# Optimization experiments

Hardware: AMD Instinct MI355X
Metric: run time of the kernel (lower is better)

The kernel has to match this reference:

```python
import jax, jax.numpy as jnp
import numpy as np

S, B, C = 7, 2, 20
D = C + 5 * B  # 30
LAMBDA_COORD = 5.0
LAMBDA_NOOBJ = 0.5
EPS = 1e-6


def _iou_yolo(b1, b2):
    # b1, b2: [..., 4] boxes in (cx, cy, w, h) 'yolo' format
    b1x1 = b1[..., 0] - b1[..., 2] / 2
    b1y1 = b1[..., 1] - b1[..., 3] / 2
    b1x2 = b1[..., 0] + b1[..., 2] / 2
    b1y2 = b1[..., 1] + b1[..., 3] / 2
    b2x1 = b2[..., 0] - b2[..., 2] / 2
    b2y1 = b2[..., 1] - b2[..., 3] / 2
    b2x2 = b2[..., 0] + b2[..., 2] / 2
    b2y2 = b2[..., 1] + b2[..., 3] / 2
    iw = jnp.clip(jnp.minimum(b1x2, b2x2) - jnp.maximum(b1x1, b2x1), 0.0)
    ih = jnp.clip(jnp.minimum(b1y2, b2y2) - jnp.maximum(b1y1, b2y1), 0.0)
    inter = iw * ih
    a1 = jnp.abs((b1x2 - b1x1) * (b1y2 - b1y1))
    a2 = jnp.abs((b2x2 - b2x1) * (b2y2 - b2y1))
    return inter / (a1 + a2 - inter + EPS)


def setup_inputs() -> dict:
    batch = 16384
    key = jax.random.key(0)
    k1, k2, k3 = jax.random.split(key, 3)
    # true coords / classes in (0.05, 0.95) so sqrt(w), sqrt(h) are well-defined
    y_trues = jax.random.uniform(k1, (batch, S, S, D), dtype=jnp.float32) * 0.9 + 0.05
    conf = (jax.random.uniform(k2, (batch, S, S)) < 0.3).astype(jnp.float32)
    y_trues = y_trues.at[..., 4].set(conf)  # objectness indicator is exactly 0 or 1
    y_preds = jax.random.normal(k3, (batch, S, S, D), dtype=jnp.float32)
    return {"y_trues": y_trues, "y_preds": y_preds}


def reference(y_trues, y_preds):
    yt = y_trues.reshape(-1, S * S, D)
    yp = y_preds.reshape(-1, S * S, D)
    batch = yt.shape[0]

    obj = (yt[..., 4] == 1.0).astype(yt.dtype)   # [N, S*S]
    noobj = 1.0 - obj

    iou1 = _iou_yolo(yt[..., 0:4], yp[..., 0:4])
    iou2 = _iou_yolo(yt[..., 0:4], yp[..., 5:9])
    best1 = iou1 > iou2                           # responsible box selection

    box_hat = jnp.where(best1[..., None], yp[..., 0:4], yp[..., 5:9])
    conf_hat = jnp.where(best1, yp[..., 4], yp[..., 9])        # responsible conf
    other_conf_hat = jnp.where(best1, yp[..., 9], yp[..., 4])  # non-responsible conf

    # xy offset loss
    xy = (yt[..., 0] - box_hat[..., 0]) ** 2 + (yt[..., 1] - box_hat[..., 1]) ** 2
    # wh loss: sqrt(true) vs sqrt(|pred + eps|)
    wh = (jnp.sqrt(yt[..., 2]) - jnp.sqrt(jnp.abs(box_hat[..., 2] + EPS))) ** 2 \
       + (jnp.sqrt(yt[..., 3]) - jnp.sqrt(jnp.abs(box_hat[..., 3] + EPS))) ** 2
    # object confidence loss (true conf == 1 in obj cells)
    obj_conf = (yt[..., 4] - conf_hat) ** 2
    # no-object penalty on the NON-responsible box inside object cells (target 0)
    noobj_in_obj = LAMBDA_NOOBJ * other_conf_hat ** 2
    # no-object penalty on BOTH boxes in cells without objects (true conf == 0)
    noobj_cells = LAMBDA_NOOBJ * ((yt[..., 4] - yp[..., 4]) ** 2
                                  + (yt[..., 4] - yp[..., 9]) ** 2)
    # class loss over C classes
    cls = jnp.sum((yt[..., 10:] - yp[..., 10:]) ** 2, axis=-1)

    per_cell = obj * (LAMBDA_COORD * (xy + wh) + obj_conf + noobj_in_obj + cls) \
             + noobj * noobj_cells
    return jnp.sum(per_cell) / batch
```

## Files before the change

### kernel.cpp

```cpp
#include <hip/hip_runtime.h>


#define SS 49
#define DD 30

__device__ __forceinline__ float iou_yolo(const float b1[4], const float b2[4]) {
    const float EPS = 1e-6f;
    float b1x1 = b1[0] - b1[2] * 0.5f, b1y1 = b1[1] - b1[3] * 0.5f;
    float b1x2 = b1[0] + b1[2] * 0.5f, b1y2 = b1[1] + b1[3] * 0.5f;
    float b2x1 = b2[0] - b2[2] * 0.5f, b2y1 = b2[1] - b2[3] * 0.5f;
    float b2x2 = b2[0] + b2[2] * 0.5f, b2y2 = b2[1] + b2[3] * 0.5f;
    float iw = fmaxf(fminf(b1x2, b2x2) - fmaxf(b1x1, b2x1), 0.0f);
    float ih = fmaxf(fminf(b1y2, b2y2) - fmaxf(b1y1, b2y1), 0.0f);
    float inter = iw * ih;
    float a1 = fabsf((b1x2 - b1x1) * (b1y2 - b1y1));
    float a2 = fabsf((b2x2 - b2x1) * (b2y2 - b2y1));
    return inter / (a1 + a2 - inter + EPS);
}

__global__ __launch_bounds__(256)
void yolo_loss_kernel(const float* __restrict__ yt_g,
                      const float* __restrict__ yp_g,
                      float* __restrict__ out,
                      int ncells, float inv_batch) {
    const float LAMBDA_COORD = 5.0f;
    const float LAMBDA_NOOBJ = 0.5f;
    const float EPS = 1e-6f;

    int cell = blockIdx.x * blockDim.x + threadIdx.x;
    float per_cell = 0.0f;

    if (cell < ncells) {
        const float2* yt2 = reinterpret_cast<const float2*>(yt_g + (size_t)cell * DD);
        const float2* yp2 = reinterpret_cast<const float2*>(yp_g + (size_t)cell * DD);
        float yt[DD], yp[DD];
#pragma unroll
        for (int i = 0; i < DD / 2; ++i) {
            float2 a = yt2[i]; yt[2 * i] = a.x; yt[2 * i + 1] = a.y;
            float2 b = yp2[i]; yp[2 * i] = b.x; yp[2 * i + 1] = b.y;
        }

        float obj = (yt[4] == 1.0f) ? 1.0f : 0.0f;
        float noobj = 1.0f - obj;

        float iou1 = iou_yolo(&yt[0], &yp[0]);
        float iou2 = iou_yolo(&yt[0], &yp[5]);
        bool best1 = iou1 > iou2;

        float bh0 = best1 ? yp[0] : yp[5];
        float bh1 = best1 ? yp[1] : yp[6];
        float bh2 = best1 ? yp[2] : yp[7];
        float bh3 = best1 ? yp[3] : yp[8];
        float conf_hat       = best1 ? yp[4] : yp[9];
        float other_conf_hat = best1 ? yp[9] : yp[4];

        float dx = yt[0] - bh0, dy = yt[1] - bh1;
        float xy = dx * dx + dy * dy;

        float sw = sqrtf(yt[2]) - sqrtf(fabsf(bh2 + EPS));
        float sh = sqrtf(yt[3]) - sqrtf(fabsf(bh3 + EPS));
        float wh = sw * sw + sh * sh;

        float dc = yt[4] - conf_hat;
        float obj_conf = dc * dc;

        float noobj_in_obj = LAMBDA_NOOBJ * other_conf_hat * other_conf_hat;

        float d4 = yt[4] - yp[4];
        float d9 = yt[4] - yp[9];
        float noobj_cells = LAMBDA_NOOBJ * (d4 * d4 + d9 * d9);

        float cls = 0.0f;
#pragma unroll
        for (int k = 10; k < DD; ++k) {
            float d = yt[k] - yp[k];
            cls += d * d;
        }

        per_cell = obj * (LAMBDA_COORD * (xy + wh) + obj_conf + noobj_in_obj + cls)
                 + noobj * noobj_cells;
    }

#pragma unroll
    for (int off = 32; off > 0; off >>= 1)
        per_cell += __shfl_down(per_cell, off, 64);

    __shared__ float smem[4];
    int lane = threadIdx.x & 63;
    int wave = threadIdx.x >> 6;
    if (lane == 0) smem[wave] = per_cell;
    __syncthreads();
    if (threadIdx.x == 0) {
        float s = smem[0] + smem[1] + smem[2] + smem[3];
        atomicAdd(out, s * inv_batch);
    }
}

extern "C" void kernel_launch(void* const* d_in, const int* in_sizes, int n_in,
                              void* d_out, int out_size, void* d_ws, size_t ws_size,
                              hipStream_t stream) {
    const float* yt = (const float*)d_in[0];
    const float* yp = (const float*)d_in[1];
    float* out = (float*)d_out;

    int total = in_sizes[0];
    int ncells = total / DD;
    int batch = ncells / SS;

    hipMemsetAsync(out, 0, sizeof(float), stream);

    int block = 256;
    int grid = (ncells + block - 1) / block;
    yolo_loss_kernel<<<grid, block, 0, stream>>>(yt, yp, out, ncells, 1.0f / (float)batch);
}
```

Measured before the change: 211.7 us.

## Stage cell tiles into LDS with coalesced direct global-to-LDS loads

Each block now copies its contiguous tile of 256 cells for both inputs into shared memory using 16-byte global_load_lds transfers, then each thread reads its cell's 30 floats from LDS. Previously each thread issued strided float2 loads at a 120-byte stride, which coalesce poorly. The cost is 60 KB of LDS per block, which limits occupancy, an extra barrier, and LDS bank conflicts from the stride-30 per-thread reads.

```diff
diff --git a/kernel.cpp b/kernel.cpp
--- a/kernel.cpp
+++ b/kernel.cpp
@@ -3,6 +3,16 @@
 
 #define SS 49
 #define DD 30
+#define BLOCK 256
+#define CPB 256
+#define TILE_F (CPB * DD)
+
+__device__ __forceinline__ void g2l16(const float* g, float* l) {
+    __builtin_amdgcn_global_load_lds(
+        (const __attribute__((address_space(1))) void*)g,
+        (__attribute__((address_space(3))) void*)l,
+        16, 0, 0);
+}
 
 __device__ __forceinline__ float iou_yolo(const float b1[4], const float b2[4]) {
     const float EPS = 1e-6f;
@@ -18,7 +28,7 @@
     return inter / (a1 + a2 - inter + EPS);
 }
 
-__global__ __launch_bounds__(256)
+__global__ __launch_bounds__(BLOCK)
 void yolo_loss_kernel(const float* __restrict__ yt_g,
                       const float* __restrict__ yp_g,
                       float* __restrict__ out,
@@ -27,24 +37,42 @@
     const float LAMBDA_NOOBJ = 0.5f;
     const float EPS = 1e-6f;
 
-    int cell = blockIdx.x * blockDim.x + threadIdx.x;
+    __shared__ __align__(16) float lt[TILE_F];
+    __shared__ __align__(16) float lp[TILE_F];
+
+    const int tid = threadIdx.x;
+    const int base_cell = blockIdx.x * CPB;
+    const int nc = min(CPB, ncells - base_cell);
+    const int nf = nc * DD;
+    const int nf4 = nf >> 2;
+    const size_t base_f = (size_t)base_cell * DD;
+
+    const float* gt = yt_g + base_f;
+    const float* gp = yp_g + base_f;
+
+    for (int j = tid; j < nf4; j += BLOCK) {
+        g2l16(gt + 4 * j, &lt[4 * j]);
+        g2l16(gp + 4 * j, &lp[4 * j]);
+    }
+    for (int j = (nf4 << 2) + tid; j < nf; j += BLOCK) {
+        lt[j] = gt[j];
+        lp[j] = gp[j];
+    }
+    __syncthreads();
+
     float per_cell = 0.0f;
-
-    if (cell < ncells) {
-        const float2* yt2 = reinterpret_cast<const float2*>(yt_g + (size_t)cell * DD);
-        const float2* yp2 = reinterpret_cast<const float2*>(yp_g + (size_t)cell * DD);
-        float yt[DD], yp[DD];
-#pragma unroll
-        for (int i = 0; i < DD / 2; ++i) {
-            float2 a = yt2[i]; yt[2 * i] = a.x; yt[2 * i + 1] = a.y;
-            float2 b = yp2[i]; yp[2 * i] = b.x; yp[2 * i + 1] = b.y;
-        }
+    if (tid < nc) {
+        const float* yt = &lt[tid * DD];
+        const float* yp = &lp[tid * DD];
 
         float obj = (yt[4] == 1.0f) ? 1.0f : 0.0f;
         float noobj = 1.0f - obj;
 
-        float iou1 = iou_yolo(&yt[0], &yp[0]);
-        float iou2 = iou_yolo(&yt[0], &yp[5]);
+        float tb[4] = {yt[0], yt[1], yt[2], yt[3]};
+        float pb1[4] = {yp[0], yp[1], yp[2], yp[3]};
+        float pb2[4] = {yp[5], yp[6], yp[7], yp[8]};
+        float iou1 = iou_yolo(tb, pb1);
+        float iou2 = iou_yolo(tb, pb2);
         bool best1 = iou1 > iou2;
 
         float bh0 = best1 ? yp[0] : yp[5];
@@ -85,7 +113,7 @@
     for (int off = 32; off > 0; off >>= 1)
         per_cell += __shfl_down(per_cell, off, 64);
 
-    __shared__ float smem[4];
+    __shared__ float smem[BLOCK / 64];
     int lane = threadIdx.x & 63;
     int wave = threadIdx.x >> 6;
     if (lane == 0) smem[wave] = per_cell;
@@ -109,7 +137,7 @@
 
     hipMemsetAsync(out, 0, sizeof(float), stream);
 
-    int block = 256;
-    int grid = (ncells + block - 1) / block;
-    yolo_loss_kernel<<<grid, block, 0, stream>>>(yt, yp, out, ncells, 1.0f / (float)batch);
+    int grid = (ncells + CPB - 1) / CPB;
+    yolo_loss_kernel<<<grid, BLOCK, 0, stream>>>(yt, yp, out, ncells,
+                                                 1.0f / (float)batch);
 }
```

After: 204.9 us. -3.2%, faster.
